# Kernel tuning notes

Measured on AMD Instinct MI355X. Metric: run time of the kernel, lower is better.

Reference implementation:

```python
import jax, jax.numpy as jnp
import numpy as np

N = 16_777_216  # number of patients / flattened timesteps


def setup_inputs() -> dict:
    key = jax.random.key(0)
    k1, k2, k3, k4, k5 = jax.random.split(key, 5)
    predictions = jax.random.uniform(k1, (N,), dtype=jnp.float32)
    targets = jax.random.randint(k2, (N,), 0, 2).astype(jnp.float32)
    sepsis_flags = jax.random.randint(k3, (N,), 0, 2, dtype=jnp.int32)
    sepsis_times = jax.random.uniform(k4, (N,), dtype=jnp.float32) * 200.0
    current_times = jax.random.uniform(k5, (N,), dtype=jnp.float32) * 200.0
    return {
        "predictions": predictions,
        "targets": targets,
        "sepsis_flags": sepsis_flags,
        "sepsis_times": sepsis_times,
        "current_times": current_times,
    }


def reference(predictions, targets, sepsis_flags, sepsis_times, current_times):
    # Hard-coded utility-function constants from UtilityLoss.__init__
    dt_early = -12.0
    dt_optimal = -6.0
    dt_late = 3.0
    max_u_tp = 1.0
    min_u_fn = -2.0
    u_fp = -0.05
    u_tn = 0.0
    m_1 = max_u_tp / (dt_optimal - dt_early)
    b_1 = -m_1 * dt_early
    m_2 = -max_u_tp / (dt_late - dt_optimal)
    b_2 = -m_2 * dt_late
    m_3 = min_u_fn / (dt_late - dt_optimal)
    b_3 = -m_3 * dt_optimal

    f = sepsis_flags.astype(predictions.dtype)
    septic = sepsis_flags > 0

    # t_sepsis = sepsis_times - dt_optimal; d = t - t_sepsis
    d = current_times - (sepsis_times - dt_optimal)
    in_win = d <= dt_late       # t <= t_sepsis + dt_late
    early = d <= dt_optimal     # t <= t_sepsis + dt_optimal

    u_TP = jnp.where(
        in_win & septic,
        jnp.where(early, jnp.maximum(m_1 * d + b_1, u_fp), m_2 * d + b_2),
        0.0,
    )
    u_FN = jnp.where(
        in_win & septic,
        jnp.where(early, 0.0, m_3 * d + b_3),
        0.0,
    )
    u_FP = jnp.where(in_win, u_fp, 0.0)
    u_TN = jnp.where(in_win, u_tn, 0.0)  # u_tn == 0, kept for fidelity

    u_func = predictions * (u_TP * f + u_FP * (1.0 - f)) + (1.0 - predictions) * (
        u_FN * f + u_TN * (1.0 - f)
    )
    return jnp.sum(-u_func)
```

## Files before the change

### kernel.cpp

```cpp
#include <hip/hip_runtime.h>

#define BLOCK 256
#define GRID 2048

__device__ __forceinline__ float util_elem(float p, int flag, float s, float c) {
    float d = c - s - 6.0f;
    if (d > 3.0f) return 0.0f;
    float u;
    if (flag) {
        float uTP, uFN;
        if (d <= -6.0f) {
            uTP = fmaxf(fmaf(d, 1.0f / 6.0f, 2.0f), -0.05f);
            uFN = 0.0f;
        } else {
            uTP = fmaf(d, -1.0f / 9.0f, 1.0f / 3.0f);
            uFN = fmaf(d, -2.0f / 9.0f, -4.0f / 3.0f);
        }
        u = p * uTP + (1.0f - p) * uFN;
    } else {
        u = p * -0.05f;
    }
    return u;
}

__device__ __forceinline__ float block_reduce_sum(float v) {
    __shared__ float smem[BLOCK / 64];
    #pragma unroll
    for (int o = 32; o > 0; o >>= 1) v += __shfl_down(v, o, 64);
    int lane = threadIdx.x & 63;
    int wid  = threadIdx.x >> 6;
    if (lane == 0) smem[wid] = v;
    __syncthreads();
    if (wid == 0) {
        v = (lane < BLOCK / 64) ? smem[lane] : 0.0f;
        #pragma unroll
        for (int o = (BLOCK / 64) / 2; o > 0; o >>= 1) v += __shfl_down(v, o, 64);
    }
    return v;
}

__global__ __launch_bounds__(BLOCK) void util_partial(
    const float4* __restrict__ pred, const int4* __restrict__ flg,
    const float4* __restrict__ ts,   const float4* __restrict__ tc,
    float* __restrict__ partials, int n4) {
    float acc = 0.0f;
    int stride = gridDim.x * blockDim.x;
    for (int i = blockIdx.x * blockDim.x + threadIdx.x; i < n4; i += stride) {
        float4 p = pred[i];
        int4   f = flg[i];
        float4 s = ts[i];
        float4 c = tc[i];
        acc += util_elem(p.x, f.x, s.x, c.x);
        acc += util_elem(p.y, f.y, s.y, c.y);
        acc += util_elem(p.z, f.z, s.z, c.z);
        acc += util_elem(p.w, f.w, s.w, c.w);
    }
    float bsum = block_reduce_sum(acc);
    if (threadIdx.x == 0) partials[blockIdx.x] = bsum;
}

__global__ __launch_bounds__(BLOCK) void util_final(
    const float* __restrict__ partials, float* __restrict__ out, int n) {
    float v = 0.0f;
    for (int i = threadIdx.x; i < n; i += BLOCK) v += partials[i];
    float total = block_reduce_sum(v);
    if (threadIdx.x == 0) out[0] = -total;
}

extern "C" void kernel_launch(void* const* d_in, const int* in_sizes, int n_in,
                              void* d_out, int out_size, void* d_ws, size_t ws_size,
                              hipStream_t stream) {
    const float4* pred = (const float4*)d_in[0];
    const int4*   flg  = (const int4*)d_in[2];
    const float4* ts   = (const float4*)d_in[3];
    const float4* tc   = (const float4*)d_in[4];

    int n  = in_sizes[0];
    int n4 = n / 4;

    float* partials = (float*)d_ws;
    float* out = (float*)d_out;

    util_partial<<<GRID, BLOCK, 0, stream>>>(pred, flg, ts, tc, partials, n4);
    util_final<<<1, BLOCK, 0, stream>>>(partials, out, GRID);
}
```

Baseline: 48.91 us.

## Fuse final reduction via last-block atomic counter and unroll loads by two

Replaces the separate final-reduction kernel with a last-block-done pattern: each block writes its partial, bumps an atomic counter, and the last block sums all partials and writes the result. The grid-stride loop is also unrolled by two so each thread has two sets of vector loads in flight. This removes one kernel launch but adds a memset of the counter on the stream, plus threadfences and an atomic per block.

```diff
diff --git a/kernel.cpp b/kernel.cpp
--- a/kernel.cpp
+++ b/kernel.cpp
@@ -23,6 +23,14 @@
     return u;
 }
 
+__device__ __forceinline__ float quad_sum(float4 p, int4 f, float4 s, float4 c) {
+    float a = util_elem(p.x, f.x, s.x, c.x);
+    a += util_elem(p.y, f.y, s.y, c.y);
+    a += util_elem(p.z, f.z, s.z, c.z);
+    a += util_elem(p.w, f.w, s.w, c.w);
+    return a;
+}
+
 __device__ __forceinline__ float block_reduce_sum(float v) {
     __shared__ float smem[BLOCK / 64];
     #pragma unroll
@@ -39,32 +47,44 @@
     return v;
 }
 
-__global__ __launch_bounds__(BLOCK) void util_partial(
+__global__ __launch_bounds__(BLOCK) void util_fused(
     const float4* __restrict__ pred, const int4* __restrict__ flg,
     const float4* __restrict__ ts,   const float4* __restrict__ tc,
-    float* __restrict__ partials, int n4) {
+    float* __restrict__ partials, unsigned int* __restrict__ ctr,
+    float* __restrict__ out, int n4) {
     float acc = 0.0f;
     int stride = gridDim.x * blockDim.x;
-    for (int i = blockIdx.x * blockDim.x + threadIdx.x; i < n4; i += stride) {
-        float4 p = pred[i];
-        int4   f = flg[i];
-        float4 s = ts[i];
-        float4 c = tc[i];
-        acc += util_elem(p.x, f.x, s.x, c.x);
-        acc += util_elem(p.y, f.y, s.y, c.y);
-        acc += util_elem(p.z, f.z, s.z, c.z);
-        acc += util_elem(p.w, f.w, s.w, c.w);
+    int base = blockIdx.x * blockDim.x + threadIdx.x;
+
+    int i = base;
+    for (; i + stride < n4; i += 2 * stride) {
+        int j = i + stride;
+        float4 p0 = pred[i]; int4 f0 = flg[i]; float4 s0 = ts[i]; float4 c0 = tc[i];
+        float4 p1 = pred[j]; int4 f1 = flg[j]; float4 s1 = ts[j]; float4 c1 = tc[j];
+        acc += quad_sum(p0, f0, s0, c0);
+        acc += quad_sum(p1, f1, s1, c1);
     }
+    if (i < n4) {
+        acc += quad_sum(pred[i], flg[i], ts[i], tc[i]);
+    }
+
     float bsum = block_reduce_sum(acc);
-    if (threadIdx.x == 0) partials[blockIdx.x] = bsum;
-}
 
-__global__ __launch_bounds__(BLOCK) void util_final(
-    const float* __restrict__ partials, float* __restrict__ out, int n) {
-    float v = 0.0f;
-    for (int i = threadIdx.x; i < n; i += BLOCK) v += partials[i];
-    float total = block_reduce_sum(v);
-    if (threadIdx.x == 0) out[0] = -total;
+    __shared__ bool is_last;
+    if (threadIdx.x == 0) {
+        partials[blockIdx.x] = bsum;
+        __threadfence();
+        unsigned int prev = atomicAdd(ctr, 1u);
+        is_last = (prev == gridDim.x - 1);
+    }
+    __syncthreads();
+    if (is_last) {
+        __threadfence();
+        float v = 0.0f;
+        for (int k = threadIdx.x; k < gridDim.x; k += BLOCK) v += partials[k];
+        float total = block_reduce_sum(v);
+        if (threadIdx.x == 0) out[0] = -total;
+    }
 }
 
 extern "C" void kernel_launch(void* const* d_in, const int* in_sizes, int n_in,
@@ -78,9 +98,11 @@
     int n  = in_sizes[0];
     int n4 = n / 4;
 
-    float* partials = (float*)d_ws;
-    float* out = (float*)d_out;
+    float*        partials = (float*)d_ws;
+    unsigned int* ctr      = (unsigned int*)((char*)d_ws + GRID * sizeof(float));
+    float*        out      = (float*)d_out;
 
-    util_partial<<<GRID, BLOCK, 0, stream>>>(pred, flg, ts, tc, partials, n4);
-    util_final<<<1, BLOCK, 0, stream>>>(partials, out, GRID);
+    hipMemsetAsync(ctr, 0, sizeof(unsigned int), stream);
+
+    util_fused<<<GRID, BLOCK, 0, stream>>>(pred, flg, ts, tc, partials, ctr, out, n4);
 }
```

Result: slower. 114.5 us (+134.1%).
